# Kernel optimization log

Measured on AMD Instinct MI355X. Metric: run time of the kernel, lower is better.

## Reference

```python
import jax, jax.numpy as jnp
import numpy as np

B, S, D = 4, 2048, 1024
H, DK, DV = 16, 64, 64


def setup_inputs() -> dict:
    key = jax.random.key(0)
    kx, kq, kk, kv, ko = jax.random.split(key, 5)
    scale = 0.02
    return {
        "x": jax.random.normal(kx, (B, S, D), dtype=jnp.float32),
        "Wq": jax.random.normal(kq, (H, D, DK), dtype=jnp.float32) * scale,
        "Wk": jax.random.normal(kk, (H, D, DK), dtype=jnp.float32) * scale,
        "Wv": jax.random.normal(kv, (H, D, DV), dtype=jnp.float32) * scale,
        "Wo": jax.random.normal(ko, (H * DV, D), dtype=jnp.float32) * scale,
    }


def reference(x, Wq, Wk, Wv, Wo):
    # Per-head projections, batched over heads with einsum (same math as
    # the original per-head Linear loop).
    q = jnp.einsum("bsd,hdk->bhsk", x, Wq)  # [B,H,S,DK]
    k = jnp.einsum("bsd,hdk->bhsk", x, Wk)  # [B,H,S,DK]
    v = jnp.einsum("bsd,hdv->bhsv", x, Wv)  # [B,H,S,DV]

    scores = jnp.einsum("bhqk,bhsk->bhqs", q, k) / jnp.sqrt(
        jnp.asarray(DK, dtype=x.dtype)
    )  # [B,H,S,S]
    # Causal mask: position q attends only to s <= q.
    causal = jnp.tril(jnp.ones((S, S), dtype=bool))
    scores = jnp.where(causal, scores, jnp.asarray(-1e9, dtype=scores.dtype))
    attn = jax.nn.softmax(scores, axis=-1)

    ctx = jnp.einsum("bhqs,bhsv->bhqv", attn, v)  # [B,H,S,DV]
    # Concat heads: [B,S,H*DV], then output projection (no bias).
    ctx = ctx.transpose(0, 2, 1, 3).reshape(B, S, H * DV)
    return ctx @ Wo  # [B,S,D]
```

## Files before the change

### kernel.cpp

```cpp
#include <hip/hip_runtime.h>
#include <hip/hip_bf16.h>

#define SB 2048
#define DM 1024
#define NH 16
#define HD 64
#define BB 4
#define MTOT (BB * SB)

typedef __attribute__((ext_vector_type(8))) short bf16x8;
typedef __attribute__((ext_vector_type(4))) short bf16x4;
typedef __attribute__((ext_vector_type(4))) float f32x4;
typedef __attribute__((ext_vector_type(4))) __fp16 f16x4;
typedef __attribute__((ext_vector_type(2))) __fp16 f16x2;

__device__ __forceinline__ short f2bf(float f) {
    union { float f; unsigned u; } a; a.f = f;
    unsigned r = (a.u + 0x7FFF + ((a.u >> 16) & 1)) >> 16;
    return (short)r;
}

__global__ __launch_bounds__(256) void cvt_x(const float* __restrict__ in,
                                             short* __restrict__ out) {
    const int i = (blockIdx.x * 256 + threadIdx.x) * 8;
    float4 v0 = *(const float4*)(in + i);
    float4 v1 = *(const float4*)(in + i + 4);
    bf16x8 o = { f2bf(v0.x), f2bf(v0.y), f2bf(v0.z), f2bf(v0.w),
                 f2bf(v1.x), f2bf(v1.y), f2bf(v1.z), f2bf(v1.w) };
    *(bf16x8*)(out + i) = o;
}

__global__ __launch_bounds__(256) void cvt_wT(const float* __restrict__ in,
                                              short* __restrict__ out,
                                              int R, int C) {
    __shared__ float Ls[64][65];
    const int tilesC = C >> 6, tilesR = R >> 6;
    const int bid = blockIdx.x;
    const int b = bid / (tilesR * tilesC);
    const int rem = bid % (tilesR * tilesC);
    const int R0 = (rem / tilesC) << 6;
    const int C0 = (rem % tilesC) << 6;
    const float* src = in + (size_t)b * R * C;
    short* dst = out + (size_t)b * R * C;
    const int t = threadIdx.x;
    const int r = t >> 2, c4 = (t & 3) << 4;
    const float* p = src + (size_t)(R0 + r) * C + C0 + c4;
#pragma unroll
    for (int u = 0; u < 16; u += 4) {
        float4 v = *(const float4*)(p + u);
        Ls[r][c4 + u] = v.x; Ls[r][c4 + u + 1] = v.y;
        Ls[r][c4 + u + 2] = v.z; Ls[r][c4 + u + 3] = v.w;
    }
    __syncthreads();
    const int cc = t >> 2, u2 = (t & 3) << 4;
    short* q = dst + (size_t)(C0 + cc) * R + R0 + u2;
    bf16x8 o0, o1;
#pragma unroll
    for (int j = 0; j < 8; ++j) o0[j] = f2bf(Ls[u2 + j][cc]);
#pragma unroll
    for (int j = 0; j < 8; ++j) o1[j] = f2bf(Ls[u2 + 8 + j][cc]);
    *(bf16x8*)(q) = o0;
    *(bf16x8*)(q + 8) = o1;
}

template <int MODE>
__global__ __launch_bounds__(256) void mm_bf16(const short* __restrict__ A,
                                               const short* __restrict__ BT,
                                               short* __restrict__ qO,
                                               short* __restrict__ kO,
                                               _Float16* __restrict__ vO,
                                               float* __restrict__ fO) {
    __shared__ short sA[128 * 32];
    __shared__ short sB[128 * 32];
    const int t = threadIdx.x;
    const int lane = t & 63;
    const int w = t >> 6;
    const int wm = w >> 1, wn = w & 1;
    const int l15 = lane & 15, quad = lane >> 4;
    const int m0 = blockIdx.x * 128;
    const int n0 = blockIdx.y * 128;

    f32x4 acc[4][4] = {};
    const int row0 = t >> 2;
    const int kc = (t & 3) * 8;

    for (int k0 = 0; k0 < DM; k0 += 32) {
#pragma unroll
        for (int u = 0; u < 2; ++u) {
            const short* ga = A + (size_t)(m0 + u * 64 + row0) * DM + k0 + kc;
            const short* gb = BT + (size_t)(n0 + u * 64 + row0) * DM + k0 + kc;
            __builtin_amdgcn_global_load_lds(
                (const __attribute__((address_space(1))) unsigned*)ga,
                (__attribute__((address_space(3))) unsigned*)&sA[(u * 64 + row0) * 32 + kc],
                16, 0, 0);
            __builtin_amdgcn_global_load_lds(
                (const __attribute__((address_space(1))) unsigned*)gb,
                (__attribute__((address_space(3))) unsigned*)&sB[(u * 64 + row0) * 32 + kc],
                16, 0, 0);
        }
        __syncthreads();

        bf16x8 af[4], bfr[4];
#pragma unroll
        for (int i = 0; i < 4; ++i) {
            af[i]  = *(const bf16x8*)&sA[(wm * 64 + i * 16 + l15) * 32 + quad * 8];
            bfr[i] = *(const bf16x8*)&sB[(wn * 64 + i * 16 + l15) * 32 + quad * 8];
        }
#pragma unroll
        for (int i = 0; i < 4; ++i)
#pragma unroll
            for (int j = 0; j < 4; ++j) {
                if (MODE == 2)
                    acc[i][j] = __builtin_amdgcn_mfma_f32_16x16x32_bf16(af[i], bfr[j],
                                                                        acc[i][j], 0, 0, 0);
                else
                    acc[i][j] = __builtin_amdgcn_mfma_f32_16x16x32_bf16(bfr[j], af[i],
                                                                        acc[i][j], 0, 0, 0);
            }
        __syncthreads();
    }

    if (MODE == 2) {
#pragma unroll
        for (int i = 0; i < 4; ++i) {
            const int m = m0 + wm * 64 + i * 16 + quad * 4;
            const int b = m >> 11, s0 = m & (SB - 1);
#pragma unroll
            for (int j = 0; j < 4; ++j) {
                const int n = n0 + wn * 64 + j * 16 + l15;
                const int h = n >> 6, d = n & 63;
                f16x2 a = __builtin_amdgcn_cvt_pkrtz(acc[i][j][0], acc[i][j][1]);
                f16x2 b2 = __builtin_amdgcn_cvt_pkrtz(acc[i][j][2], acc[i][j][3]);
                f16x4 o = {a.x, a.y, b2.x, b2.y};
                *(f16x4*)&vO[((size_t)((b * NH + h) * HD + d)) * SB + s0] = o;
            }
        }
    } else {
#pragma unroll
        for (int i = 0; i < 4; ++i) {
            const int m = m0 + wm * 64 + i * 16 + l15;
            const int b = m >> 11, s = m & (SB - 1);
#pragma unroll
            for (int j = 0; j < 4; ++j) {
                const int n = n0 + wn * 64 + j * 16 + quad * 4;
                if (MODE == 1) {
                    f32x4 v = acc[i][j];
                    *(float4*)&fO[(size_t)m * DM + n] = *(float4*)&v;
                } else {
                    const int seg = n >> 10;
                    const int h = (n & 1023) >> 6, d0 = n & 63;
                    const float sc = (seg == 0) ? 0.125f : 1.0f;
                    bf16x4 o;
#pragma unroll
                    for (int r = 0; r < 4; ++r) o[r] = f2bf(acc[i][j][r] * sc);
                    short* dst = (seg == 0) ? qO : kO;
                    *(bf16x4*)&dst[(((size_t)(b * NH + h) * SB + s) << 6) + d0] = o;
                }
            }
        }
    }
}

__global__ __launch_bounds__(256) void attn_mfma(const short* __restrict__ Q,
                                                 const short* __restrict__ K,
                                                 const _Float16* __restrict__ VT,
                                                 short* __restrict__ ctx) {
    __shared__ short    sK[2][64 * 64];
    __shared__ _Float16 sV[2][64 * 64];

    const int t = threadIdx.x;
    const int lane = t & 63, w = t >> 6;
    const int l15 = lane & 15, quad = lane >> 4;
    const int idx = blockIdx.x;
    const int bh = ((idx >> 6) << 3) | (idx & 7);
    const int pair = (idx >> 3) & 7;
    const int b = bh >> 4, h = bh & 15;
    const size_t hb = (size_t)bh * SB * HD;
    const short* Qb = Q + hb;
    const short* Kb = K + hb;
    const _Float16* Vb = VT + hb;

    const int srow = t >> 3;
    const int sch  = t & 7;
    const int srow2 = srow + 32;
    const int swl = l15 & 7;

    auto stage = [&](int k0, int bbuf) {
        __builtin_amdgcn_global_load_lds(
            (const __attribute__((address_space(1))) unsigned*)
                (Kb + (size_t)(k0 + srow) * HD + ((sch ^ (srow & 7)) << 3)),
            (__attribute__((address_space(3))) unsigned*)&sK[bbuf][t << 3], 16, 0, 0);
        __builtin_amdgcn_global_load_lds(
            (const __attribute__((address_space(1))) unsigned*)
                (Kb + (size_t)(k0 + srow2) * HD + ((sch ^ (srow2 & 7)) << 3)),
            (__attribute__((address_space(3))) unsigned*)&sK[bbuf][(t + 256) << 3], 16, 0, 0);
        __builtin_amdgcn_global_load_lds(
            (const __attribute__((address_space(1))) unsigned*)
                (Vb + (size_t)srow * SB + k0 + ((sch ^ (srow & 7)) << 3)),
            (__attribute__((address_space(3))) unsigned*)&sV[bbuf][t << 3], 16, 0, 0);
        __builtin_amdgcn_global_load_lds(
            (const __attribute__((address_space(1))) unsigned*)
                (Vb + (size_t)srow2 * SB + k0 + ((sch ^ (srow2 & 7)) << 3)),
            (__attribute__((address_space(3))) unsigned*)&sV[bbuf][(t + 256) << 3], 16, 0, 0);
    };

#pragma unroll
    for (int ph = 0; ph < 2; ++ph) {
        const int qt = ph ? (15 - pair) : pair;
        const int q0 = qt * 128;
        const int qw = q0 + w * 32;

        bf16x8 aq[2][2];
#pragma unroll
        for (int qg = 0; qg < 2; ++qg)
#pragma unroll
            for (int hh = 0; hh < 2; ++hh)
                aq[qg][hh] = *(const bf16x8*)(Qb + (size_t)(qw + qg * 16 + l15) * HD +
                                              hh * 32 + quad * 8);

        f32x4 O[2][4] = {};
        float l_r[2] = {0.f, 0.f};
        const int Tw = qw >> 6;
        const int Tblk = 2 * qt + 1;

        stage(0, 0);

        for (int kt = 0; kt <= Tblk; ++kt) {
            __syncthreads();
            if (kt < Tblk) stage((kt + 1) * 64, (kt + 1) & 1);
            if (kt > Tw) continue;

            const int buf = kt & 1;
            const int k0 = kt * 64;
            const bool diag = (kt == Tw);
            const short* sKb = &sK[buf][0];
            const _Float16* sVb = &sV[buf][0];

            f32x4 sc[2][4] = {};
#pragma unroll
            for (int st = 0; st < 4; ++st) {
                const int row = st * 16 + l15;
#pragma unroll
                for (int hh = 0; hh < 2; ++hh) {
                    bf16x8 kf = *(const bf16x8*)&sKb[(row << 6) +
                                                     (((hh * 4 + quad) ^ swl) << 3)];
                    sc[0][st] = __builtin_amdgcn_mfma_f32_16x16x32_bf16(kf, aq[0][hh], sc[0][st], 0, 0, 0);
                    sc[1][st] = __builtin_amdgcn_mfma_f32_16x16x32_bf16(kf, aq[1][hh], sc[1][st], 0, 0, 0);
                }
            }

#pragma unroll
            for (int st = 0; st < 4; ++st) {
                const int s0 = k0 + st * 16;
                if (diag && s0 > qw + 31) break;
                f16x4 vf[4];
                const int vch = ((st * 2 + (quad >> 1)) ^ swl) << 3;
#pragma unroll
                for (int dj = 0; dj < 4; ++dj)
                    vf[dj] = *(const f16x4*)&sVb[((dj * 16 + l15) << 6) + vch + (quad & 1) * 4];
#pragma unroll
                for (int qg = 0; qg < 2; ++qg) {
                    const int qmin = qw + qg * 16;
                    if (diag && s0 > qmin + 15) continue;
                    float p[4];
                    if (!diag || s0 + 15 <= qmin) {
#pragma unroll
                        for (int r = 0; r < 4; ++r) p[r] = __expf(sc[qg][st][r]);
                    } else {
#pragma unroll
                        for (int r = 0; r < 4; ++r) {
                            const int sg = s0 + quad * 4 + r;
                            p[r] = (sg <= qmin + l15) ? __expf(sc[qg][st][r]) : 0.f;
                        }
                    }
                    l_r[qg] += (p[0] + p[1]) + (p[2] + p[3]);
                    f16x2 pa = __builtin_amdgcn_cvt_pkrtz(p[0], p[1]);
                    f16x2 pb = __builtin_amdgcn_cvt_pkrtz(p[2], p[3]);
                    f16x4 pf = {pa.x, pa.y, pb.x, pb.y};
#pragma unroll
                    for (int dj = 0; dj < 4; ++dj)
                        O[qg][dj] = __builtin_amdgcn_mfma_f32_16x16x16f16(vf[dj], pf,
                                                                          O[qg][dj], 0, 0, 0);
                }
            }
        }

#pragma unroll
        for (int qg = 0; qg < 2; ++qg) {
            float l = l_r[qg];
            l += __shfl_xor(l, 16);
            l += __shfl_xor(l, 32);
            const float inv = 1.f / l;
            const int q = qw + qg * 16 + l15;
#pragma unroll
            for (int dj = 0; dj < 4; ++dj) {
                bf16x4 o;
#pragma unroll
                for (int r = 0; r < 4; ++r) o[r] = f2bf(O[qg][dj][r] * inv);
                *(bf16x4*)&ctx[(size_t)(b * SB + q) * DM + h * HD + dj * 16 + quad * 4] = o;
            }
        }
    }
}

extern "C" void kernel_launch(void* const* d_in, const int* in_sizes, int n_in,
                              void* d_out, int out_size, void* d_ws, size_t ws_size,
                              hipStream_t stream) {
    const float* x  = (const float*)d_in[0];
    const float* Wq = (const float*)d_in[1];
    const float* Wk = (const float*)d_in[2];
    const float* Wv = (const float*)d_in[3];
    const float* Wo = (const float*)d_in[4];
    float* out = (float*)d_out;

    const size_t NX = (size_t)MTOT * DM;
    const size_t NW = (size_t)DM * DM;
    short* xb   = (short*)d_ws;
    short* wall = xb + NX;
    short* wot  = wall + 3 * NW;
    short* qb   = wot + NW;
    short* kb   = qb + NX;
    short* vtb  = kb + NX;
    short* ctxb = vtb + NX;

    dim3 blk(256);
    cvt_x<<<NX / (256 * 8), blk, 0, stream>>>(x, xb);
    cvt_wT<<<16 * 16, blk, 0, stream>>>(Wq, wall, DM, HD);
    cvt_wT<<<16 * 16, blk, 0, stream>>>(Wk, wall + NW, DM, HD);
    cvt_wT<<<16 * 16, blk, 0, stream>>>(Wv, wall + 2 * NW, DM, HD);
    cvt_wT<<<16 * 16, blk, 0, stream>>>(Wo, wot, DM, DM);

    dim3 gqk(MTOT / 128, 2048 / 128);
    mm_bf16<0><<<gqk, blk, 0, stream>>>(xb, wall, qb, kb, nullptr, nullptr);
    dim3 gv(MTOT / 128, 1024 / 128);
    mm_bf16<2><<<gv, blk, 0, stream>>>(xb, wall + 2 * NW, nullptr, nullptr,
                                       (_Float16*)vtb, nullptr);

    attn_mfma<<<dim3(512), blk, 0, stream>>>(qb, kb, (const _Float16*)vtb, ctxb);

    dim3 gout(MTOT / 128, DM / 128);
    mm_bf16<1><<<gout, blk, 0, stream>>>(ctxb, wot, nullptr, nullptr, nullptr, out);
}
```

Measured before the change: 285.4 us.

## Merge weight conversions and QKV GEMMs, halve attention query tile per block

Folds the four weight transpose-convert launches into one kernel and merges the Q/K and V projection GEMMs into one launch with a per-block branch on the output segment. The attention kernel now uses 64-row query tiles (16 rows per wave) instead of 128, doubling the grid to 1024 blocks with balanced causal pairing. The aim is to cut launch overhead, improve load balance and occupancy for the causal attention, and trim wasted work on diagonal tiles. In exchange each K/V tile staged in shared memory is reused by fewer query rows, and an extra barrier is added per phase.

```diff
diff --git a/kernel.cpp b/kernel.cpp
--- a/kernel.cpp
+++ b/kernel.cpp
@@ -7,6 +7,7 @@
 #define HD 64
 #define BB 4
 #define MTOT (BB * SB)
+#define NW (DM * DM)
 
 typedef __attribute__((ext_vector_type(8))) short bf16x8;
 typedef __attribute__((ext_vector_type(4))) short bf16x4;
@@ -30,16 +31,31 @@
     *(bf16x8*)(out + i) = o;
 }
 
-__global__ __launch_bounds__(256) void cvt_wT(const float* __restrict__ in,
-                                              short* __restrict__ out,
-                                              int R, int C) {
+__global__ __launch_bounds__(256) void cvt_w4(const float* __restrict__ Wq,
+                                              const float* __restrict__ Wk,
+                                              const float* __restrict__ Wv,
+                                              const float* __restrict__ Wo,
+                                              short* __restrict__ wall,
+                                              short* __restrict__ wot) {
     __shared__ float Ls[64][65];
+    const int bid = blockIdx.x;
+    const int which = bid >> 8;
+    const int rem = bid & 255;
+    const float* in;
+    short* out;
+    int R, C;
+    if (which < 3) {
+        in = (which == 0) ? Wq : (which == 1) ? Wk : Wv;
+        out = wall + (size_t)which * NW;
+        R = DM; C = HD;
+    } else {
+        in = Wo; out = wot; R = DM; C = DM;
+    }
     const int tilesC = C >> 6, tilesR = R >> 6;
-    const int bid = blockIdx.x;
-    const int b = bid / (tilesR * tilesC);
-    const int rem = bid % (tilesR * tilesC);
-    const int R0 = (rem / tilesC) << 6;
-    const int C0 = (rem % tilesC) << 6;
+    const int b = rem / (tilesR * tilesC);
+    const int rem2 = rem % (tilesR * tilesC);
+    const int R0 = (rem2 / tilesC) << 6;
+    const int C0 = (rem2 % tilesC) << 6;
     const float* src = in + (size_t)b * R * C;
     short* dst = out + (size_t)b * R * C;
     const int t = threadIdx.x;
@@ -63,13 +79,11 @@
     *(bf16x8*)(q + 8) = o1;
 }
 
-template <int MODE>
-__global__ __launch_bounds__(256) void mm_bf16(const short* __restrict__ A,
-                                               const short* __restrict__ BT,
-                                               short* __restrict__ qO,
-                                               short* __restrict__ kO,
-                                               _Float16* __restrict__ vO,
-                                               float* __restrict__ fO) {
+__global__ __launch_bounds__(256) void mm_qkv(const short* __restrict__ A,
+                                              const short* __restrict__ BT,
+                                              short* __restrict__ qO,
+                                              short* __restrict__ kO,
+                                              _Float16* __restrict__ vO) {
     __shared__ short sA[128 * 32];
     __shared__ short sB[128 * 32];
     const int t = threadIdx.x;
@@ -79,6 +93,7 @@
     const int l15 = lane & 15, quad = lane >> 4;
     const int m0 = blockIdx.x * 128;
     const int n0 = blockIdx.y * 128;
+    const bool isV = (n0 >= 2048);
 
     f32x4 acc[4][4] = {};
     const int row0 = t >> 2;
@@ -106,29 +121,33 @@
             af[i]  = *(const bf16x8*)&sA[(wm * 64 + i * 16 + l15) * 32 + quad * 8];
             bfr[i] = *(const bf16x8*)&sB[(wn * 64 + i * 16 + l15) * 32 + quad * 8];
         }
-#pragma unroll
-        for (int i = 0; i < 4; ++i)
-#pragma unroll
-            for (int j = 0; j < 4; ++j) {
-                if (MODE == 2)
+        if (isV) {
+#pragma unroll
+            for (int i = 0; i < 4; ++i)
+#pragma unroll
+                for (int j = 0; j < 4; ++j)
                     acc[i][j] = __builtin_amdgcn_mfma_f32_16x16x32_bf16(af[i], bfr[j],
                                                                         acc[i][j], 0, 0, 0);
-                else
+        } else {
+#pragma unroll
+            for (int i = 0; i < 4; ++i)
+#pragma unroll
+                for (int j = 0; j < 4; ++j)
                     acc[i][j] = __builtin_amdgcn_mfma_f32_16x16x32_bf16(bfr[j], af[i],
                                                                         acc[i][j], 0, 0, 0);
-            }
-        __syncthreads();
-    }
-
-    if (MODE == 2) {
+        }
+        __syncthreads();
+    }
+
+    if (isV) {
 #pragma unroll
         for (int i = 0; i < 4; ++i) {
             const int m = m0 + wm * 64 + i * 16 + quad * 4;
             const int b = m >> 11, s0 = m & (SB - 1);
 #pragma unroll
             for (int j = 0; j < 4; ++j) {
-                const int n = n0 + wn * 64 + j * 16 + l15;
-                const int h = n >> 6, d = n & 63;
+                const int nv = (n0 - 2048) + wn * 64 + j * 16 + l15;
+                const int h = nv >> 6, d = nv & 63;
                 f16x2 a = __builtin_amdgcn_cvt_pkrtz(acc[i][j][0], acc[i][j][1]);
                 f16x2 b2 = __builtin_amdgcn_cvt_pkrtz(acc[i][j][2], acc[i][j][3]);
                 f16x4 o = {a.x, a.y, b2.x, b2.y};
@@ -143,20 +162,75 @@
 #pragma unroll
             for (int j = 0; j < 4; ++j) {
                 const int n = n0 + wn * 64 + j * 16 + quad * 4;
-                if (MODE == 1) {
-                    f32x4 v = acc[i][j];
-                    *(float4*)&fO[(size_t)m * DM + n] = *(float4*)&v;
-                } else {
-                    const int seg = n >> 10;
-                    const int h = (n & 1023) >> 6, d0 = n & 63;
-                    const float sc = (seg == 0) ? 0.125f : 1.0f;
-                    bf16x4 o;
-#pragma unroll
-                    for (int r = 0; r < 4; ++r) o[r] = f2bf(acc[i][j][r] * sc);
-                    short* dst = (seg == 0) ? qO : kO;
-                    *(bf16x4*)&dst[(((size_t)(b * NH + h) * SB + s) << 6) + d0] = o;
-                }
+                const int seg = n >> 10;
+                const int h = (n & 1023) >> 6, d0 = n & 63;
+                const float sc = (seg == 0) ? 0.125f : 1.0f;
+                bf16x4 o;
+#pragma unroll
+                for (int r = 0; r < 4; ++r) o[r] = f2bf(acc[i][j][r] * sc);
+                short* dst = (seg == 0) ? qO : kO;
+                *(bf16x4*)&dst[(((size_t)(b * NH + h) * SB + s) << 6) + d0] = o;
             }
+        }
+    }
+}
+
+__global__ __launch_bounds__(256) void mm_out(const short* __restrict__ A,
+                                              const short* __restrict__ BT,
+                                              float* __restrict__ fO) {
+    __shared__ short sA[128 * 32];
+    __shared__ short sB[128 * 32];
+    const int t = threadIdx.x;
+    const int lane = t & 63;
+    const int w = t >> 6;
+    const int wm = w >> 1, wn = w & 1;
+    const int l15 = lane & 15, quad = lane >> 4;
+    const int m0 = blockIdx.x * 128;
+    const int n0 = blockIdx.y * 128;
+
+    f32x4 acc[4][4] = {};
+    const int row0 = t >> 2;
+    const int kc = (t & 3) * 8;
+
+    for (int k0 = 0; k0 < DM; k0 += 32) {
+#pragma unroll
+        for (int u = 0; u < 2; ++u) {
+            const short* ga = A + (size_t)(m0 + u * 64 + row0) * DM + k0 + kc;
+            const short* gb = BT + (size_t)(n0 + u * 64 + row0) * DM + k0 + kc;
+            __builtin_amdgcn_global_load_lds(
+                (const __attribute__((address_space(1))) unsigned*)ga,
+                (__attribute__((address_space(3))) unsigned*)&sA[(u * 64 + row0) * 32 + kc],
+                16, 0, 0);
+            __builtin_amdgcn_global_load_lds(
+                (const __attribute__((address_space(1))) unsigned*)gb,
+                (__attribute__((address_space(3))) unsigned*)&sB[(u * 64 + row0) * 32 + kc],
+                16, 0, 0);
+        }
+        __syncthreads();
+
+        bf16x8 af[4], bfr[4];
+#pragma unroll
+        for (int i = 0; i < 4; ++i) {
+            af[i]  = *(const bf16x8*)&sA[(wm * 64 + i * 16 + l15) * 32 + quad * 8];
+            bfr[i] = *(const bf16x8*)&sB[(wn * 64 + i * 16 + l15) * 32 + quad * 8];
+        }
+#pragma unroll
+        for (int i = 0; i < 4; ++i)
+#pragma unroll
+            for (int j = 0; j < 4; ++j)
+                acc[i][j] = __builtin_amdgcn_mfma_f32_16x16x32_bf16(bfr[j], af[i],
+                                                                    acc[i][j], 0, 0, 0);
+        __syncthreads();
+    }
+
+#pragma unroll
+    for (int i = 0; i < 4; ++i) {
+        const int m = m0 + wm * 64 + i * 16 + l15;
+#pragma unroll
+        for (int j = 0; j < 4; ++j) {
+            const int n = n0 + wn * 64 + j * 16 + quad * 4;
+            f32x4 v = acc[i][j];
+            *(float4*)&fO[(size_t)m * DM + n] = *(float4*)&v;
         }
     }
 }
@@ -172,8 +246,8 @@
     const int lane = t & 63, w = t >> 6;
     const int l15 = lane & 15, quad = lane >> 4;
     const int idx = blockIdx.x;
-    const int bh = ((idx >> 6) << 3) | (idx & 7);
-    const int pair = (idx >> 3) & 7;
+    const int bh = ((idx >> 7) << 3) | (idx & 7);
+    const int pair = (idx >> 3) & 15;
     const int b = bh >> 4, h = bh & 15;
     const size_t hb = (size_t)bh * SB * HD;
     const short* Qb = Q + hb;
@@ -206,37 +280,30 @@
 
 #pragma unroll
     for (int ph = 0; ph < 2; ++ph) {
-        const int qt = ph ? (15 - pair) : pair;
-        const int q0 = qt * 128;
-        const int qw = q0 + w * 32;
-
-        bf16x8 aq[2][2];
-#pragma unroll
-        for (int qg = 0; qg < 2; ++qg)
-#pragma unroll
-            for (int hh = 0; hh < 2; ++hh)
-                aq[qg][hh] = *(const bf16x8*)(Qb + (size_t)(qw + qg * 16 + l15) * HD +
-                                              hh * 32 + quad * 8);
-
-        f32x4 O[2][4] = {};
-        float l_r[2] = {0.f, 0.f};
-        const int Tw = qw >> 6;
-        const int Tblk = 2 * qt + 1;
-
+        const int qt = ph ? (31 - pair) : pair;
+        const int qw = qt * 64 + w * 16;
+
+        bf16x8 aq[2];
+#pragma unroll
+        for (int hh = 0; hh < 2; ++hh)
+            aq[hh] = *(const bf16x8*)(Qb + (size_t)(qw + l15) * HD + hh * 32 + quad * 8);
+
+        f32x4 O[4] = {};
+        float l_r = 0.f;
+
+        __syncthreads();
         stage(0, 0);
 
-        for (int kt = 0; kt <= Tblk; ++kt) {
+        for (int kt = 0; kt <= qt; ++kt) {
             __syncthreads();
-            if (kt < Tblk) stage((kt + 1) * 64, (kt + 1) & 1);
-            if (kt > Tw) continue;
+            if (kt < qt) stage((kt + 1) * 64, (kt + 1) & 1);
 
             const int buf = kt & 1;
-            const int k0 = kt * 64;
-            const bool diag = (kt == Tw);
+            const bool diag = (kt == qt);
             const short* sKb = &sK[buf][0];
             const _Float16* sVb = &sV[buf][0];
 
-            f32x4 sc[2][4] = {};
+            f32x4 sc[4] = {};
 #pragma unroll
             for (int st = 0; st < 4; ++st) {
                 const int row = st * 16 + l15;
@@ -244,61 +311,48 @@
                 for (int hh = 0; hh < 2; ++hh) {
                     bf16x8 kf = *(const bf16x8*)&sKb[(row << 6) +
                                                      (((hh * 4 + quad) ^ swl) << 3)];
-                    sc[0][st] = __builtin_amdgcn_mfma_f32_16x16x32_bf16(kf, aq[0][hh], sc[0][st], 0, 0, 0);
-                    sc[1][st] = __builtin_amdgcn_mfma_f32_16x16x32_bf16(kf, aq[1][hh], sc[1][st], 0, 0, 0);
+                    sc[st] = __builtin_amdgcn_mfma_f32_16x16x32_bf16(kf, aq[hh], sc[st], 0, 0, 0);
                 }
             }
 
 #pragma unroll
             for (int st = 0; st < 4; ++st) {
-                const int s0 = k0 + st * 16;
-                if (diag && s0 > qw + 31) break;
+                if (diag && st > w) break;
                 f16x4 vf[4];
                 const int vch = ((st * 2 + (quad >> 1)) ^ swl) << 3;
 #pragma unroll
                 for (int dj = 0; dj < 4; ++dj)
                     vf[dj] = *(const f16x4*)&sVb[((dj * 16 + l15) << 6) + vch + (quad & 1) * 4];
-#pragma unroll
-                for (int qg = 0; qg < 2; ++qg) {
-                    const int qmin = qw + qg * 16;
-                    if (diag && s0 > qmin + 15) continue;
-                    float p[4];
-                    if (!diag || s0 + 15 <= qmin) {
-#pragma unroll
-                        for (int r = 0; r < 4; ++r) p[r] = __expf(sc[qg][st][r]);
-                    } else {
-#pragma unroll
-                        for (int r = 0; r < 4; ++r) {
-                            const int sg = s0 + quad * 4 + r;
-                            p[r] = (sg <= qmin + l15) ? __expf(sc[qg][st][r]) : 0.f;
-                        }
-                    }
-                    l_r[qg] += (p[0] + p[1]) + (p[2] + p[3]);
-                    f16x2 pa = __builtin_amdgcn_cvt_pkrtz(p[0], p[1]);
-                    f16x2 pb = __builtin_amdgcn_cvt_pkrtz(p[2], p[3]);
-                    f16x4 pf = {pa.x, pa.y, pb.x, pb.y};
-#pragma unroll
-                    for (int dj = 0; dj < 4; ++dj)
-                        O[qg][dj] = __builtin_amdgcn_mfma_f32_16x16x16f16(vf[dj], pf,
-                                                                          O[qg][dj], 0, 0, 0);
+                float p[4];
+                if (!diag || st < w) {
+#pragma unroll
+                    for (int r = 0; r < 4; ++r) p[r] = __expf(sc[st][r]);
+                } else {
+#pragma unroll
+                    for (int r = 0; r < 4; ++r)
+                        p[r] = (quad * 4 + r <= l15) ? __expf(sc[st][r]) : 0.f;
                 }
+                l_r += (p[0] + p[1]) + (p[2] + p[3]);
+                f16x2 pa = __builtin_amdgcn_cvt_pkrtz(p[0], p[1]);
+                f16x2 pb = __builtin_amdgcn_cvt_pkrtz(p[2], p[3]);
+                f16x4 pf = {pa.x, pa.y, pb.x, pb.y};
+#pragma unroll
+                for (int dj = 0; dj < 4; ++dj)
+                    O[dj] = __builtin_amdgcn_mfma_f32_16x16x16f16(vf[dj], pf, O[dj], 0, 0, 0);
             }
         }
 
-#pragma unroll
-        for (int qg = 0; qg < 2; ++qg) {
-            float l = l_r[qg];
-            l += __shfl_xor(l, 16);
-            l += __shfl_xor(l, 32);
-            const float inv = 1.f / l;
-            const int q = qw + qg * 16 + l15;
-#pragma unroll
-            for (int dj = 0; dj < 4; ++dj) {
-                bf16x4 o;
-#pragma unroll
-                for (int r = 0; r < 4; ++r) o[r] = f2bf(O[qg][dj][r] * inv);
-                *(bf16x4*)&ctx[(size_t)(b * SB + q) * DM + h * HD + dj * 16 + quad * 4] = o;
-            }
+        float l = l_r;
+        l += __shfl_xor(l, 16);
+        l += __shfl_xor(l, 32);
+        const float inv = 1.f / l;
+        const int q = qw + l15;
+#pragma unroll
+        for (int dj = 0; dj < 4; ++dj) {
+            bf16x4 o;
+#pragma unroll
+            for (int r = 0; r < 4; ++r) o[r] = f2bf(O[dj][r] * inv);
+            *(bf16x4*)&ctx[(size_t)(b * SB + q) * DM + h * HD + dj * 16 + quad * 4] = o;
         }
     }
 }
@@ -314,10 +368,9 @@
     float* out = (float*)d_out;
 
     const size_t NX = (size_t)MTOT * DM;
-    const size_t NW = (size_t)DM * DM;
     short* xb   = (short*)d_ws;
     short* wall = xb + NX;
-    short* wot  = wall + 3 * NW;
+    short* wot  = wall + 3 * (size_t)NW;
     short* qb   = wot + NW;
     short* kb   = qb + NX;
     short* vtb  = kb + NX;
@@ -325,19 +378,13 @@
 
     dim3 blk(256);
     cvt_x<<<NX / (256 * 8), blk, 0, stream>>>(x, xb);
-    cvt_wT<<<16 * 16, blk, 0, stream>>>(Wq, wall, DM, HD);
-    cvt_wT<<<16 * 16, blk, 0, stream>>>(Wk, wall + NW, DM, HD);
-    cvt_wT<<<16 * 16, blk, 0, stream>>>(Wv, wall + 2 * NW, DM, HD);
-    cvt_wT<<<16 * 16, blk, 0, stream>>>(Wo, wot, DM, DM);
-
-    dim3 gqk(MTOT / 128, 2048 / 128);
-    mm_bf16<0><<<gqk, blk, 0, stream>>>(xb, wall, qb, kb, nullptr, nullptr);
-    dim3 gv(MTOT / 128, 1024 / 128);
-    mm_bf16<2><<<gv, blk, 0, stream>>>(xb, wall + 2 * NW, nullptr, nullptr,
-                                       (_Float16*)vtb, nullptr);
-
-    attn_mfma<<<dim3(512), blk, 0, stream>>>(qb, kb, (const _Float16*)vtb, ctxb);
+    cvt_w4<<<1024, blk, 0, stream>>>(Wq, Wk, Wv, Wo, wall, wot);
+
+    dim3 gqkv(MTOT / 128, 3072 / 128);
+    mm_qkv<<<gqkv, blk, 0, stream>>>(xb, wall, qb, kb, (_Float16*)vtb);
+
+    attn_mfma<<<dim3(1024), blk, 0, stream>>>(qb, kb, (const _Float16*)vtb, ctxb);
 
     dim3 gout(MTOT / 128, DM / 128);
-    mm_bf16<1><<<gout, blk, 0, stream>>>(ctxb, wot, nullptr, nullptr, nullptr, out);
-}
+    mm_out<<<gout, blk, 0, stream>>>(ctxb, wot, out);
+}
```

Result: faster. 263.2 us (-7.8%).
